# Kernel optimization log

Measured on AMD Instinct MI355X. Metric: run time of the kernel, lower is better.

## Reference

```python
import jax, jax.numpy as jnp
import numpy as np

B, P, PD = 32, 196, 768          # batch, n_subdivs, subdiv feature dim
D, H, L, NC = 768, 12, 8, 1000   # n_dims, n_heads, n_blocks, n_classes
HD = D // H                      # per-head dim (64)


def _pos_emb(n_pos, d):
    # faithful to _sinusoidal_positional_embeddings: row i (timestep) parity picks sin/cos
    i = jnp.arange(n_pos, dtype=jnp.float32)[:, None]
    j = jnp.arange(d, dtype=jnp.float32)[None, :]
    sin_v = jnp.sin(i / jnp.power(10000.0, j / d))
    cos_v = jnp.cos(i / jnp.power(10000.0, (j - 1.0) / d))
    return jnp.where((jnp.arange(n_pos)[:, None] % 2) == 0, sin_v, cos_v)  # (n_pos, d)


def _layernorm(x, g, b, eps=1e-5):
    m = jnp.mean(x, axis=-1, keepdims=True)
    v = jnp.var(x, axis=-1, keepdims=True)
    return (x - m) * jax.lax.rsqrt(v + eps) * g + b


def setup_inputs() -> dict:
    key = jax.random.key(0)
    ks = iter(jax.random.split(key, 16))
    nrm = lambda shape, s=0.02: jax.random.normal(next(ks), shape, jnp.float32) * s
    return {
        "x": jax.random.normal(next(ks), (B, P, PD), jnp.float32),
        "W_emb": nrm((PD, D)), "b_emb": jnp.zeros((D,), jnp.float32),
        "v_class": jax.random.uniform(next(ks), (1, D), jnp.float32),
        "ln1_g": jnp.ones((L, D), jnp.float32), "ln1_b": jnp.zeros((L, D), jnp.float32),
        "Wq": nrm((L, H, HD, HD)), "bq": jnp.zeros((L, H, HD), jnp.float32),
        "Wk": nrm((L, H, HD, HD)), "bk": jnp.zeros((L, H, HD), jnp.float32),
        "Wv": nrm((L, H, HD, HD)), "bv": jnp.zeros((L, H, HD), jnp.float32),
        "ln2_g": jnp.ones((L, D), jnp.float32), "ln2_b": jnp.zeros((L, D), jnp.float32),
        "W1": nrm((L, D, 4 * D)), "b1": jnp.zeros((L, 4 * D), jnp.float32),
        "W2": nrm((L, 4 * D, D)), "b2": jnp.zeros((L, D), jnp.float32),
        "W_cls": nrm((D, NC)), "b_cls": jnp.zeros((NC,), jnp.float32),
    }


def reference(x, W_emb, b_emb, v_class, ln1_g, ln1_b, Wq, bq, Wk, bk, Wv, bv,
              ln2_g, ln2_b, W1, b1, W2, b2, W_cls, b_cls):
    b = x.shape[0]
    pos = _pos_emb(P, D)                                  # (P, D), same for every sample
    h = x @ W_emb + b_emb + pos                           # (B, P, D)
    cls_tok = jnp.broadcast_to(v_class[None], (b, 1, D))
    h = jnp.concatenate([cls_tok, h], axis=1)             # (B, S, D), S = P + 1
    S = P + 1
    attns = []
    for l in range(L):
        # --- MHSA: each head reads only its own hd-slice of the input ---
        xn = _layernorm(h, ln1_g[l], ln1_b[l])
        xh = xn.reshape(b, S, H, HD)
        q = jnp.einsum('bshi,hij->bshj', xh, Wq[l]) + bq[l]
        k = jnp.einsum('bshi,hij->bshj', xh, Wk[l]) + bk[l]
        v = jnp.einsum('bshi,hij->bshj', xh, Wv[l]) + bv[l]
        scores = jnp.einsum('bqhj,bkhj->bhqk', q, k) / (HD ** 0.5)
        a = jax.nn.softmax(scores, axis=-1)               # (B, H, S, S)
        attns.append(jnp.mean(a, axis=1))                 # mean over heads, (B, S, S)
        o = jnp.einsum('bhqk,bkhj->bqhj', a, v).reshape(b, S, D)
        h = o + h                                         # residual 1
        # --- MLP ---
        xn2 = _layernorm(h, ln2_g[l], ln2_b[l])
        m = jax.nn.gelu(xn2 @ W1[l] + b1[l], approximate=False)
        h = m @ W2[l] + b2[l] + h                         # residual 2
    cls = h[:, 0]
    pred = jax.nn.softmax(cls @ W_cls + b_cls, axis=-1)   # (B, NC)
    return pred, jnp.stack(attns)                         # attns: (L, B, S, S)
```

## Files before the change

### kernel.cpp

```cpp
#include <hip/hip_runtime.h>
#include <cstdint>

typedef unsigned short u16;
typedef __attribute__((ext_vector_type(8))) short bf16x8;
typedef __attribute__((ext_vector_type(4))) float f32x4;

#define DEV static __device__ __forceinline__

#define BB 32
#define PP 196
#define DD 768
#define HH 12
#define HDD 64
#define SS 197
#define NTOK 6304
#define NTOKX 6272
#define NCLS 1000
#define DD4 3072
#define KPAD 224
#define NBH 384
#define NLAY 8

DEV u16 f2bf(float f){ unsigned u=__float_as_uint(f); u += 0x7FFFu + ((u>>16)&1u); return (u16)(u>>16); }
DEV float bf2f(u16 u){ return __uint_as_float(((unsigned)u)<<16); }

typedef __attribute__((address_space(1))) void gas1;
typedef __attribute__((address_space(3))) void las3;

DEV void gld16(const void* g, void* l){
  __builtin_amdgcn_global_load_lds((gas1*)(uintptr_t)g, (las3*)(unsigned)(uintptr_t)l, 16, 0, 0);
}

struct __align__(8) u16x4 { u16 x,y,z,w; };


__global__ void pos_kernel(float* __restrict__ pos){
  int idx = blockIdx.x*256 + threadIdx.x;
  if (idx >= PP*DD) return;
  int p = idx / DD, j = idx - p*DD;
  int odd = p & 1;
  float e = ((float)j - (float)odd) * (1.0f/(float)DD);
  float arg = (float)p / powf(10000.0f, e);
  pos[idx] = odd ? cosf(arg) : sinf(arg);
}

__global__ void f32_to_bf16_kernel(const float* __restrict__ in, u16* __restrict__ out, int n4){
  int i = blockIdx.x*256 + threadIdx.x;
  if (i >= n4) return;
  float4 v = reinterpret_cast<const float4*>(in)[i];
  u16x4 o = { f2bf(v.x), f2bf(v.y), f2bf(v.z), f2bf(v.w) };
  reinterpret_cast<u16x4*>(out)[i] = o;
}

__global__ void clstok_kernel(const float* __restrict__ vcls, float* __restrict__ h){
  int b = blockIdx.x;
  for (int i = threadIdx.x; i < DD; i += 256)
    h[(size_t)b*SS*DD + i] = vcls[i];
}

__global__ void transpose_kernel(const float* __restrict__ in, u16* __restrict__ out, int R, int C){
  __shared__ float tile[32][33];
  int bx = blockIdx.x*32, by = blockIdx.y*32;
  size_t zoff = (size_t)blockIdx.z * R * C;
  const float* src = in + zoff;
  u16* dst = out + zoff;
  int tx = threadIdx.x, ty = threadIdx.y;
  #pragma unroll
  for (int q=0;q<4;q++)
    tile[ty + q*8][tx] = src[(size_t)(by + ty + q*8)*C + bx + tx];
  __syncthreads();
  #pragma unroll
  for (int q=0;q<4;q++)
    dst[(size_t)(bx + ty + q*8)*R + by + tx] = f2bf(tile[tx][ty + q*8]);
}

__global__ void ln_kernel(const float* __restrict__ h, const float* __restrict__ g,
                          const float* __restrict__ b, u16* __restrict__ xn){
  int t = blockIdx.x*4 + (threadIdx.x>>6);
  int lane = threadIdx.x & 63;
  const float4* src = reinterpret_cast<const float4*>(h + (size_t)t*DD);
  float4 xv[3];
  float s = 0.f, s2 = 0.f;
  #pragma unroll
  for (int p=0;p<3;p++){
    xv[p] = src[p*64 + lane];
    s  += xv[p].x + xv[p].y + xv[p].z + xv[p].w;
    s2 += xv[p].x*xv[p].x + xv[p].y*xv[p].y + xv[p].z*xv[p].z + xv[p].w*xv[p].w;
  }
  #pragma unroll
  for (int o=32;o>0;o>>=1){ s += __shfl_xor(s,o); s2 += __shfl_xor(s2,o); }
  float mean = s * (1.f/(float)DD);
  float rstd = rsqrtf(s2*(1.f/(float)DD) - mean*mean + 1e-5f);
  #pragma unroll
  for (int p=0;p<3;p++){
    int base = p*256 + lane*4;
    u16x4 o4 = { f2bf((xv[p].x-mean)*rstd*g[base+0]+b[base+0]),
                 f2bf((xv[p].y-mean)*rstd*g[base+1]+b[base+1]),
                 f2bf((xv[p].z-mean)*rstd*g[base+2]+b[base+2]),
                 f2bf((xv[p].w-mean)*rstd*g[base+3]+b[base+3]) };
    *reinterpret_cast<u16x4*>(&xn[(size_t)t*DD + base]) = o4;
  }
}

template<int EPI>
__global__ __launch_bounds__(256) void gemm_bf16(
    const u16* __restrict__ A, const u16* __restrict__ BT, int M, int K,
    int nbm, int nbn,
    const float* __restrict__ bias, const float* __restrict__ pos,
    float* __restrict__ Hout, u16* __restrict__ Bout)
{
  __shared__ __align__(16) u16 As[3][128*32];
  __shared__ __align__(16) u16 Bs[3][128*32];
  const int tid = threadIdx.x;
  const int wave = tid>>6, lane = tid&63;

  const int nwg = nbm*nbn;
  const int wg = blockIdx.x;
  const int xcd = wg & 7, ii = wg >> 3;
  const int q8 = nwg >> 3, r8 = nwg & 7;
  const int lin = (xcd < r8 ? xcd*(q8+1) : r8*(q8+1) + (xcd-r8)*q8) + ii;
  const int bm = lin / nbn, bn = lin - bm*nbn;

  const int wr = wave>>1, wc = wave&1;

  f32x4 acc[4][4] = {};

  const int lr = lane>>2;
  const int lc = ((lane&3) ^ ((lane>>3)&3)) * 8;
  int ar0 = bm*128 + (wave*2+0)*16 + lr; if (ar0 > M-1) ar0 = M-1;
  int ar1 = bm*128 + (wave*2+1)*16 + lr; if (ar1 > M-1) ar1 = M-1;
  const u16* aS0 = A + (size_t)ar0*K + lc;
  const u16* aS1 = A + (size_t)ar1*K + lc;
  const u16* bS0 = BT + (size_t)(bn*128 + (wave*2+0)*16 + lr)*K + lc;
  const u16* bS1 = BT + (size_t)(bn*128 + (wave*2+1)*16 + lr)*K + lc;
  const int d0 = (wave*2+0)*512;
  const int d1 = (wave*2+1)*512;

  auto stage = [&](int buf, int kt){
    gld16(aS0 + kt, &As[buf][d0]);
    gld16(aS1 + kt, &As[buf][d1]);
    gld16(bS0 + kt, &Bs[buf][d0]);
    gld16(bS1 + kt, &Bs[buf][d1]);
  };
  const int rchunk = ((lane>>4) ^ (((lane&15)>>1)&3)) * 8;
  auto compute = [&](int buf){
    bf16x8 af[4], bfv[4];
    #pragma unroll
    for (int i=0;i<4;i++)
      af[i] = *reinterpret_cast<const bf16x8*>(&As[buf][(wr*64 + i*16 + (lane&15))*32 + rchunk]);
    #pragma unroll
    for (int j=0;j<4;j++)
      bfv[j] = *reinterpret_cast<const bf16x8*>(&Bs[buf][(wc*64 + j*16 + (lane&15))*32 + rchunk]);
    #pragma unroll
    for (int i=0;i<4;i++)
      #pragma unroll
      for (int j=0;j<4;j++)
        acc[i][j] = __builtin_amdgcn_mfma_f32_16x16x32_bf16(af[i], bfv[j], acc[i][j], 0, 0, 0);
  };

  const int NT = K >> 5;
  stage(0, 0);
  stage(1, 32);
  for (int t = 0; t < NT-2; ++t){
    asm volatile("s_waitcnt vmcnt(4)" ::: "memory");
    __builtin_amdgcn_s_barrier();
    __builtin_amdgcn_sched_barrier(0);
    stage((t+2)%3, (t+2)*32);
    compute(t%3);
  }
  asm volatile("s_waitcnt vmcnt(4)" ::: "memory");
  __builtin_amdgcn_s_barrier();
  __builtin_amdgcn_sched_barrier(0);
  compute((NT-2)%3);
  asm volatile("s_waitcnt vmcnt(0)" ::: "memory");
  __builtin_amdgcn_s_barrier();
  __builtin_amdgcn_sched_barrier(0);
  compute((NT-1)%3);

  const int rowb = bm*128 + wr*64 + (lane>>4)*4;
  const int colb = bn*128 + wc*64 + (lane&15);
  const int Nst = nbn * 128;
  #pragma unroll
  for (int i=0;i<4;i++){
    #pragma unroll
    for (int j=0;j<4;j++){
      int col = colb + j*16;
      #pragma unroll
      for (int r=0;r<4;r++){
        int row = rowb + i*16 + r;
        if (row >= M) continue;
        float v = acc[i][j][r];
        if (EPI == 0){
          int bb = row / PP, p = row - bb*PP;
          Hout[((size_t)(bb*SS + 1 + p))*DD + col] = v + bias[col] + pos[p*DD + col];
        } else if (EPI == 1){
          float xg = v + bias[col];
          Bout[(size_t)row*Nst + col] = f2bf(0.5f*xg*(1.f + erff(xg*0.7071067811865475f)));
        } else {
          Hout[(size_t)row*DD + col] += v + bias[col];
        }
      }
    }
  }
}

__global__ __launch_bounds__(256) void qkv_kernel(
    const u16* __restrict__ xn,
    const u16* __restrict__ WqT, const u16* __restrict__ WkT, const u16* __restrict__ WvT,
    const float* __restrict__ bq, const float* __restrict__ bk, const float* __restrict__ bv,
    u16* __restrict__ qb, u16* __restrict__ kb, u16* __restrict__ vb)
{
  const int LDA = 72;
  __shared__ __align__(16) u16 Asm[128*72];
  __shared__ __align__(16) u16 Wsm[3][64*72];
  const int tid = threadIdx.x, wave = tid>>6, lane = tid&63;
  const int bm = blockIdx.x, hd = blockIdx.y;

  #pragma unroll
  for (int ps=0; ps<4; ++ps){
    int e = (ps*256 + tid)*8;
    int row = e>>6, col = e&63;
    int gr = bm*128 + row; if (gr > NTOK-1) gr = NTOK-1;
    *reinterpret_cast<int4*>(&Asm[row*LDA + col]) =
        *reinterpret_cast<const int4*>(&xn[(size_t)gr*DD + hd*HDD + col]);
  }
  const u16* wsrc[3] = { WqT + hd*4096, WkT + hd*4096, WvT + hd*4096 };
  #pragma unroll
  for (int w=0; w<3; ++w)
    #pragma unroll
    for (int ps=0; ps<2; ++ps){
      int e = (ps*256 + tid)*8;
      int row = e>>6, col = e&63;
      *reinterpret_cast<int4*>(&Wsm[w][row*LDA + col]) =
          *reinterpret_cast<const int4*>(&wsrc[w][row*64 + col]);
    }
  __syncthreads();

  bf16x8 af[2][2];
  #pragma unroll
  for (int i=0;i<2;i++)
    #pragma unroll
    for (int kk=0;kk<2;kk++)
      af[i][kk] = *reinterpret_cast<const bf16x8*>(&Asm[(wave*32 + i*16 + (lane&15))*LDA + kk*32 + (lane>>4)*8]);

  f32x4 acc[3][2][4] = {};
  #pragma unroll
  for (int w=0;w<3;w++)
    #pragma unroll
    for (int kk=0;kk<2;kk++)
      #pragma unroll
      for (int j=0;j<4;j++){
        bf16x8 bfv = *reinterpret_cast<const bf16x8*>(&Wsm[w][(j*16 + (lane&15))*LDA + kk*32 + (lane>>4)*8]);
        #pragma unroll
        for (int i=0;i<2;i++)
          acc[w][i][j] = __builtin_amdgcn_mfma_f32_16x16x32_bf16(af[i][kk], bfv, acc[w][i][j], 0,0,0);
      }

  const float* bqh = bq + hd*HDD;
  const float* bkh = bk + hd*HDD;
  const float* bvh = bv + hd*HDD;
  #pragma unroll
  for (int i=0;i<2;i++)
    #pragma unroll
    for (int j=0;j<4;j++){
      int d = j*16 + (lane&15);
      #pragma unroll
      for (int r=0;r<4;r++){
        int t = bm*128 + wave*32 + i*16 + (lane>>4)*4 + r;
        if (t >= NTOK) continue;
        int b = t / SS, sx = t - b*SS;
        size_t bh = (size_t)b*HH + hd;
        qb[(bh*SS + sx)*HDD + d] = f2bf(acc[0][i][j][r] + bqh[d]);
        kb[(bh*SS + sx)*HDD + d] = f2bf(acc[1][i][j][r] + bkh[d]);
        vb[(bh*KPAD + sx)*HDD + d] = f2bf(acc[2][i][j][r] + bvh[d]);
      }
    }
}

__global__ __launch_bounds__(256) void scores_kernel(
    const u16* __restrict__ qb, const u16* __restrict__ kb, u16* __restrict__ sc)
{
  const int LDA = 72;
  __shared__ __align__(16) u16 Qs[128*72];
  __shared__ __align__(16) u16 Ks[128*72];
  const int tid = threadIdx.x, wave = tid>>6, lane = tid&63;
  const int bm = blockIdx.x, bn = blockIdx.y, bh = blockIdx.z;
  #pragma unroll
  for (int ps=0; ps<4; ++ps){
    int e = (ps*256 + tid)*8;
    int row = e>>6, col = e&63;
    int qr = bm*128 + row; if (qr > SS-1) qr = SS-1;
    int kr = bn*128 + row; if (kr > SS-1) kr = SS-1;
    *reinterpret_cast<int4*>(&Qs[row*LDA + col]) = *reinterpret_cast<const int4*>(&qb[((size_t)bh*SS + qr)*HDD + col]);
    *reinterpret_cast<int4*>(&Ks[row*LDA + col]) = *reinterpret_cast<const int4*>(&kb[((size_t)bh*SS + kr)*HDD + col]);
  }
  __syncthreads();
  const int wr = wave>>1, wc = wave&1;
  f32x4 acc[4][4] = {};
  #pragma unroll
  for (int kk=0;kk<2;kk++){
    bf16x8 af[4], bfv[4];
    #pragma unroll
    for (int i=0;i<4;i++) af[i] = *reinterpret_cast<const bf16x8*>(&Qs[(wr*64+i*16+(lane&15))*LDA + kk*32 + (lane>>4)*8]);
    #pragma unroll
    for (int j=0;j<4;j++) bfv[j] = *reinterpret_cast<const bf16x8*>(&Ks[(wc*64+j*16+(lane&15))*LDA + kk*32 + (lane>>4)*8]);
    #pragma unroll
    for (int i=0;i<4;i++)
      #pragma unroll
      for (int j=0;j<4;j++)
        acc[i][j] = __builtin_amdgcn_mfma_f32_16x16x32_bf16(af[i], bfv[j], acc[i][j], 0,0,0);
  }
  #pragma unroll
  for (int i=0;i<4;i++)
    #pragma unroll
    for (int j=0;j<4;j++){
      int kg = bn*128 + wc*64 + j*16 + (lane&15);
      #pragma unroll
      for (int r=0;r<4;r++){
        int qg = bm*128 + wr*64 + i*16 + (lane>>4)*4 + r;
        if (qg < SS && kg < SS)
          sc[((size_t)bh*SS + qg)*KPAD + kg] = f2bf(acc[i][j][r] * 0.125f);
      }
    }
}

__global__ void softmax_kernel(u16* __restrict__ sc){
  int row = blockIdx.x*4 + (threadIdx.x>>6);
  int lane = threadIdx.x & 63;
  u16* src = sc + (size_t)row*KPAD;
  float v[4]; float mx = -1e30f;
  #pragma unroll
  for (int p=0;p<4;p++){
    int c = lane + p*64;
    v[p] = (c < SS) ? bf2f(src[c]) : -1e30f;
    mx = fmaxf(mx, v[p]);
  }
  #pragma unroll
  for (int o=32;o>0;o>>=1) mx = fmaxf(mx, __shfl_xor(mx,o));
  float s = 0.f;
  #pragma unroll
  for (int p=0;p<4;p++){
    int c = lane + p*64;
    v[p] = (c < SS) ? expf(v[p]-mx) : 0.f;
    s += v[p];
  }
  #pragma unroll
  for (int o=32;o>0;o>>=1) s += __shfl_xor(s,o);
  float inv = 1.f / s;
  #pragma unroll
  for (int p=0;p<4;p++){
    int c = lane + p*64;
    if (c < KPAD) src[c] = f2bf((c < SS) ? v[p]*inv : 0.f);
  }
}

__global__ void attnmean_kernel(const u16* __restrict__ attn, float* __restrict__ outp){
  int qi = blockIdx.x, b = blockIdx.y, kk = threadIdx.x;
  if (kk >= SS) return;
  float s = 0.f;
  #pragma unroll
  for (int h=0; h<HH; ++h)
    s += bf2f(attn[(((size_t)b*HH + h)*SS + qi)*KPAD + kk]);
  outp[((size_t)b*SS + qi)*SS + kk] = s * (1.f/12.f);
}

__global__ __launch_bounds__(256) void av_kernel(
    const u16* __restrict__ attn, const u16* __restrict__ vb, float* __restrict__ h)
{
  const int LDA = 40;
  const int LDB = 40;
  __shared__ __align__(16) u16 Asm[128*40];
  __shared__ __align__(16) u16 Bsm[64*40];
  const int tid = threadIdx.x, wave = tid>>6, lane = tid&63;
  const int bm = blockIdx.x, bh = blockIdx.y;
  const int b = bh / HH, hd = bh - b*HH;
  f32x4 acc[2][4] = {};
  for (int k0 = 0; k0 < KPAD; k0 += 32){
    if (k0) __syncthreads();
    #pragma unroll
    for (int ps=0; ps<2; ++ps){
      int e = (ps*256 + tid)*8;
      int row = e>>5, col = e&31;
      int ar = bm*128 + row; if (ar > SS-1) ar = SS-1;
      *reinterpret_cast<int4*>(&Asm[row*LDA + col]) =
          *reinterpret_cast<const int4*>(&attn[((size_t)bh*SS + ar)*KPAD + k0 + col]);
    }
    {
      int kk = tid>>3;
      int d0 = (tid&7)*8;
      bf16x8 vv = *reinterpret_cast<const bf16x8*>(&vb[((size_t)bh*KPAD + k0 + kk)*HDD + d0]);
      #pragma unroll
      for (int q=0;q<8;q++) Bsm[(d0+q)*LDB + kk] = (u16)vv[q];
    }
    __syncthreads();
    bf16x8 af[2], bfv[4];
    #pragma unroll
    for (int i=0;i<2;i++) af[i] = *reinterpret_cast<const bf16x8*>(&Asm[(wave*32 + i*16 + (lane&15))*LDA + (lane>>4)*8]);
    #pragma unroll
    for (int j=0;j<4;j++) bfv[j] = *reinterpret_cast<const bf16x8*>(&Bsm[(j*16 + (lane&15))*LDB + (lane>>4)*8]);
    #pragma unroll
    for (int i=0;i<2;i++)
      #pragma unroll
      for (int j=0;j<4;j++)
        acc[i][j] = __builtin_amdgcn_mfma_f32_16x16x32_bf16(af[i], bfv[j], acc[i][j], 0,0,0);
  }
  #pragma unroll
  for (int i=0;i<2;i++)
    #pragma unroll
    for (int j=0;j<4;j++){
      int d = j*16 + (lane&15);
      #pragma unroll
      for (int r=0;r<4;r++){
        int sx = bm*128 + wave*32 + i*16 + (lane>>4)*4 + r;
        if (sx < SS)
          h[((size_t)b*SS + sx)*DD + hd*HDD + d] += acc[i][j][r];
      }
    }
}

__global__ __launch_bounds__(256) void logits_kernel(
    const float* __restrict__ h, const float* __restrict__ Wc,
    const float* __restrict__ bc, float* __restrict__ logits)
{
  __shared__ float xs[DD];
  const int b = blockIdx.x, tid = threadIdx.x;
  for (int i = tid; i < DD; i += 256) xs[i] = h[(size_t)b*SS*DD + i];
  __syncthreads();
  const int c = blockIdx.y*250 + tid;
  if (tid >= 250 || c >= NCLS) return;
  float acc = bc[c];
  const float* wcol = Wc + c;
  #pragma unroll 16
  for (int k = 0; k < DD; ++k)
    acc += xs[k] * wcol[(size_t)k*NCLS];
  logits[(size_t)b*NCLS + c] = acc;
}

__global__ __launch_bounds__(256) void pred_softmax_kernel(
    const float* __restrict__ logits, float* __restrict__ outp)
{
  __shared__ float red[256];
  const int b = blockIdx.x, tid = threadIdx.x;
  float acc[4], mx = -1e30f;
  #pragma unroll
  for (int m=0;m<4;m++){
    int c = tid + m*256;
    acc[m] = (c < NCLS) ? logits[(size_t)b*NCLS + c] : -1e30f;
    mx = fmaxf(mx, acc[m]);
  }
  red[tid] = mx; __syncthreads();
  for (int o=128;o>0;o>>=1){ if (tid<o) red[tid] = fmaxf(red[tid], red[tid+o]); __syncthreads(); }
  mx = red[0]; __syncthreads();
  float ex[4]; float s = 0.f;
  #pragma unroll
  for (int m=0;m<4;m++){
    int c = tid + m*256;
    ex[m] = (c < NCLS) ? expf(acc[m]-mx) : 0.f;
    s += ex[m];
  }
  red[tid] = s; __syncthreads();
  for (int o=128;o>0;o>>=1){ if (tid<o) red[tid] += red[tid+o]; __syncthreads(); }
  float inv = 1.f / red[0];
  #pragma unroll
  for (int m=0;m<4;m++){
    int c = tid + m*256;
    if (c < NCLS) outp[(size_t)b*NCLS + c] = ex[m]*inv;
  }
}

extern "C" void kernel_launch(void* const* d_in, const int* in_sizes, int n_in,
                              void* d_out, int out_size, void* d_ws, size_t ws_size,
                              hipStream_t stream)
{
  const float* x      = (const float*)d_in[0];
  const float* W_emb  = (const float*)d_in[1];
  const float* b_emb  = (const float*)d_in[2];
  const float* v_class= (const float*)d_in[3];
  const float* ln1_g  = (const float*)d_in[4];
  const float* ln1_b  = (const float*)d_in[5];
  const float* Wq     = (const float*)d_in[6];
  const float* bq     = (const float*)d_in[7];
  const float* Wk     = (const float*)d_in[8];
  const float* bk     = (const float*)d_in[9];
  const float* Wv     = (const float*)d_in[10];
  const float* bv     = (const float*)d_in[11];
  const float* ln2_g  = (const float*)d_in[12];
  const float* ln2_b  = (const float*)d_in[13];
  const float* W1     = (const float*)d_in[14];
  const float* b1     = (const float*)d_in[15];
  const float* W2     = (const float*)d_in[16];
  const float* b2     = (const float*)d_in[17];
  const float* W_cls  = (const float*)d_in[18];
  const float* b_cls  = (const float*)d_in[19];
  (void)in_sizes; (void)n_in; (void)out_size;
  float* outp = (float*)d_out;

  char* ws = (char*)d_ws;
  size_t off = 0;
  auto alloc = [&](size_t bytes)->char*{
    char* p = ws + off;
    off = (off + bytes + 255) & ~((size_t)255);
    return p;
  };
  float* pos    = (float*)alloc((size_t)PP*DD*4);
  float* hbuf   = (float*)alloc((size_t)NTOK*DD*4);
  u16*   xnb    = (u16*)  alloc((size_t)NTOK*DD*2);
  u16*   WembT  = (u16*)  alloc((size_t)DD*DD*2);
  u16*   W1Tall = (u16*)  alloc((size_t)NLAY*DD*DD4*2);
  u16*   W2Tall = (u16*)  alloc((size_t)NLAY*DD*DD4*2);
  u16*   WqT    = (u16*)  alloc((size_t)NLAY*HH*HDD*HDD*2);
  u16*   WkT    = (u16*)  alloc((size_t)NLAY*HH*HDD*HDD*2);
  u16*   WvT    = (u16*)  alloc((size_t)NLAY*HH*HDD*HDD*2);
  char*  blob   = alloc((size_t)NTOK*DD4*2);
  float* logitsb= (float*)alloc((size_t)BB*NCLS*4);
  u16* qbuf = (u16*)blob;
  u16* kbuf = qbuf + (size_t)NBH*SS*HDD;
  u16* vbuf = kbuf + (size_t)NBH*SS*HDD;
  u16* scb  = vbuf + (size_t)NBH*KPAD*HDD;
  u16* mbuf = (u16*)blob;
  u16* xbf  = scb;
  if (ws_size < off) return;

  hipMemsetAsync(vbuf, 0, (size_t)NBH*KPAD*HDD*2, stream);
  pos_kernel<<<(PP*DD+255)/256, 256, 0, stream>>>(pos);
  f32_to_bf16_kernel<<<(NTOKX*DD/4+255)/256, 256, 0, stream>>>(x, xbf, NTOKX*DD/4);
  dim3 tb(32,8);
  transpose_kernel<<<dim3(DD/32, DD/32, 1), tb, 0, stream>>>(W_emb, WembT, DD, DD);
  transpose_kernel<<<dim3(2,2,NLAY*HH), tb, 0, stream>>>(Wq, WqT, HDD, HDD);
  transpose_kernel<<<dim3(2,2,NLAY*HH), tb, 0, stream>>>(Wk, WkT, HDD, HDD);
  transpose_kernel<<<dim3(2,2,NLAY*HH), tb, 0, stream>>>(Wv, WvT, HDD, HDD);
  transpose_kernel<<<dim3(DD4/32, DD/32, NLAY), tb, 0, stream>>>(W1, W1Tall, DD, DD4);
  transpose_kernel<<<dim3(DD/32, DD4/32, NLAY), tb, 0, stream>>>(W2, W2Tall, DD4, DD);

  gemm_bf16<0><<<49*6, 256, 0, stream>>>(xbf, WembT, NTOKX, DD, 49, 6, b_emb, pos, hbuf, nullptr);
  clstok_kernel<<<BB, 256, 0, stream>>>(v_class, hbuf);

  for (int l=0; l<NLAY; ++l){
    ln_kernel<<<NTOK/4, 256, 0, stream>>>(hbuf, ln1_g + l*DD, ln1_b + l*DD, xnb);
    qkv_kernel<<<dim3(50, HH), 256, 0, stream>>>(xnb,
        WqT + (size_t)l*HH*4096, WkT + (size_t)l*HH*4096, WvT + (size_t)l*HH*4096,
        bq + l*HH*HDD, bk + l*HH*HDD, bv + l*HH*HDD, qbuf, kbuf, vbuf);
    scores_kernel<<<dim3(2,2,NBH), 256, 0, stream>>>(qbuf, kbuf, scb);
    softmax_kernel<<<NBH*SS/4, 256, 0, stream>>>(scb);
    attnmean_kernel<<<dim3(SS, BB), 256, 0, stream>>>(scb, outp + 32000 + (size_t)l*BB*SS*SS);
    av_kernel<<<dim3(2, NBH), 256, 0, stream>>>(scb, vbuf, hbuf);
    ln_kernel<<<NTOK/4, 256, 0, stream>>>(hbuf, ln2_g + l*DD, ln2_b + l*DD, xnb);
    gemm_bf16<1><<<50*24, 256, 0, stream>>>(xnb, W1Tall + (size_t)l*DD*DD4, NTOK, DD, 50, 24,
                                            b1 + l*DD4, nullptr, nullptr, mbuf);
    gemm_bf16<2><<<50*6, 256, 0, stream>>>(mbuf, W2Tall + (size_t)l*DD*DD4, NTOK, DD4, 50, 6,
                                           b2 + l*DD, nullptr, hbuf, nullptr);
  }
  logits_kernel<<<dim3(BB, 4), 256, 0, stream>>>(hbuf, W_cls, b_cls, logitsb);
  pred_softmax_kernel<<<BB, 256, 0, stream>>>(logitsb, outp);
}
```

Measured before the change: 1.957 ms.

## Fuse attention scores with softmax and switch GEMM to double-buffered LDS

The separate scores and softmax kernels are merged into one kernel. Each workgroup loads all 197 keys, computes a full row band of QK^T in registers, and applies softmax with intra-quad shuffles before writing bf16 probabilities once. This removes a bf16 round trip of the score matrix and a launch per layer. Separately, the generic GEMM goes from a 3-stage LDS pipeline to 2-stage double buffering with an extra barrier per K step. That lowers LDS use and may raise occupancy, but it risks less latency hiding.

```diff
diff --git a/kernel.cpp b/kernel.cpp
--- a/kernel.cpp
+++ b/kernel.cpp
@@ -109,8 +109,8 @@
     const float* __restrict__ bias, const float* __restrict__ pos,
     float* __restrict__ Hout, u16* __restrict__ Bout)
 {
-  __shared__ __align__(16) u16 As[3][128*32];
-  __shared__ __align__(16) u16 Bs[3][128*32];
+  __shared__ __align__(16) u16 As[2][128*32];
+  __shared__ __align__(16) u16 Bs[2][128*32];
   const int tid = threadIdx.x;
   const int wave = tid>>6, lane = tid&63;
 
@@ -160,22 +160,20 @@
 
   const int NT = K >> 5;
   stage(0, 0);
-  stage(1, 32);
-  for (int t = 0; t < NT-2; ++t){
-    asm volatile("s_waitcnt vmcnt(4)" ::: "memory");
+  int cur = 0;
+  for (int t = 0; t < NT; ++t){
+    if (t+1 < NT){
+      stage(cur^1, (t+1)*32);
+      asm volatile("s_waitcnt vmcnt(4)" ::: "memory");
+    } else {
+      asm volatile("s_waitcnt vmcnt(0)" ::: "memory");
+    }
     __builtin_amdgcn_s_barrier();
     __builtin_amdgcn_sched_barrier(0);
-    stage((t+2)%3, (t+2)*32);
-    compute(t%3);
-  }
-  asm volatile("s_waitcnt vmcnt(4)" ::: "memory");
-  __builtin_amdgcn_s_barrier();
-  __builtin_amdgcn_sched_barrier(0);
-  compute((NT-2)%3);
-  asm volatile("s_waitcnt vmcnt(0)" ::: "memory");
-  __builtin_amdgcn_s_barrier();
-  __builtin_amdgcn_sched_barrier(0);
-  compute((NT-1)%3);
+    compute(cur);
+    __builtin_amdgcn_s_barrier();
+    cur ^= 1;
+  }
 
   const int rowb = bm*128 + wr*64 + (lane>>4)*4;
   const int colb = bn*128 + wc*64 + (lane&15);
@@ -277,80 +275,91 @@
     }
 }
 
-__global__ __launch_bounds__(256) void scores_kernel(
-    const u16* __restrict__ qb, const u16* __restrict__ kb, u16* __restrict__ sc)
+__global__ __launch_bounds__(256) void attn_scores_softmax_kernel(
+    const u16* __restrict__ qb, const u16* __restrict__ kb, u16* __restrict__ attn)
 {
   const int LDA = 72;
   __shared__ __align__(16) u16 Qs[128*72];
-  __shared__ __align__(16) u16 Ks[128*72];
+  __shared__ __align__(16) u16 Ks[KPAD*72];
   const int tid = threadIdx.x, wave = tid>>6, lane = tid&63;
-  const int bm = blockIdx.x, bn = blockIdx.y, bh = blockIdx.z;
+  const int bm = blockIdx.x, bh = blockIdx.y;
+
   #pragma unroll
   for (int ps=0; ps<4; ++ps){
     int e = (ps*256 + tid)*8;
     int row = e>>6, col = e&63;
     int qr = bm*128 + row; if (qr > SS-1) qr = SS-1;
-    int kr = bn*128 + row; if (kr > SS-1) kr = SS-1;
-    *reinterpret_cast<int4*>(&Qs[row*LDA + col]) = *reinterpret_cast<const int4*>(&qb[((size_t)bh*SS + qr)*HDD + col]);
-    *reinterpret_cast<int4*>(&Ks[row*LDA + col]) = *reinterpret_cast<const int4*>(&kb[((size_t)bh*SS + kr)*HDD + col]);
+    *reinterpret_cast<int4*>(&Qs[row*LDA + col]) =
+        *reinterpret_cast<const int4*>(&qb[((size_t)bh*SS + qr)*HDD + col]);
+  }
+  #pragma unroll
+  for (int ps=0; ps<7; ++ps){
+    int e = (ps*256 + tid)*8;
+    int row = e>>6, col = e&63;
+    int kr = row; if (kr > SS-1) kr = SS-1;
+    *reinterpret_cast<int4*>(&Ks[row*LDA + col]) =
+        *reinterpret_cast<const int4*>(&kb[((size_t)bh*SS + kr)*HDD + col]);
   }
   __syncthreads();
-  const int wr = wave>>1, wc = wave&1;
-  f32x4 acc[4][4] = {};
-  #pragma unroll
-  for (int kk=0;kk<2;kk++){
-    bf16x8 af[4], bfv[4];
-    #pragma unroll
-    for (int i=0;i<4;i++) af[i] = *reinterpret_cast<const bf16x8*>(&Qs[(wr*64+i*16+(lane&15))*LDA + kk*32 + (lane>>4)*8]);
-    #pragma unroll
-    for (int j=0;j<4;j++) bfv[j] = *reinterpret_cast<const bf16x8*>(&Ks[(wc*64+j*16+(lane&15))*LDA + kk*32 + (lane>>4)*8]);
-    #pragma unroll
-    for (int i=0;i<4;i++)
-      #pragma unroll
-      for (int j=0;j<4;j++)
-        acc[i][j] = __builtin_amdgcn_mfma_f32_16x16x32_bf16(af[i], bfv[j], acc[i][j], 0,0,0);
-  }
-  #pragma unroll
-  for (int i=0;i<4;i++)
-    #pragma unroll
-    for (int j=0;j<4;j++){
-      int kg = bn*128 + wc*64 + j*16 + (lane&15);
-      #pragma unroll
-      for (int r=0;r<4;r++){
-        int qg = bm*128 + wr*64 + i*16 + (lane>>4)*4 + r;
-        if (qg < SS && kg < SS)
-          sc[((size_t)bh*SS + qg)*KPAD + kg] = f2bf(acc[i][j][r] * 0.125f);
-      }
-    }
-}
-
-__global__ void softmax_kernel(u16* __restrict__ sc){
-  int row = blockIdx.x*4 + (threadIdx.x>>6);
-  int lane = threadIdx.x & 63;
-  u16* src = sc + (size_t)row*KPAD;
-  float v[4]; float mx = -1e30f;
-  #pragma unroll
-  for (int p=0;p<4;p++){
-    int c = lane + p*64;
-    v[p] = (c < SS) ? bf2f(src[c]) : -1e30f;
-    mx = fmaxf(mx, v[p]);
-  }
-  #pragma unroll
-  for (int o=32;o>0;o>>=1) mx = fmaxf(mx, __shfl_xor(mx,o));
-  float s = 0.f;
-  #pragma unroll
-  for (int p=0;p<4;p++){
-    int c = lane + p*64;
-    v[p] = (c < SS) ? expf(v[p]-mx) : 0.f;
-    s += v[p];
-  }
-  #pragma unroll
-  for (int o=32;o>0;o>>=1) s += __shfl_xor(s,o);
-  float inv = 1.f / s;
-  #pragma unroll
-  for (int p=0;p<4;p++){
-    int c = lane + p*64;
-    if (c < KPAD) src[c] = f2bf((c < SS) ? v[p]*inv : 0.f);
+
+  bf16x8 af[2][2];
+  #pragma unroll
+  for (int i=0;i<2;i++)
+    #pragma unroll
+    for (int kk=0;kk<2;kk++)
+      af[i][kk] = *reinterpret_cast<const bf16x8*>(&Qs[(wave*32 + i*16 + (lane&15))*LDA + kk*32 + (lane>>4)*8]);
+
+  f32x4 acc[2][14];
+  #pragma unroll
+  for (int i=0;i<2;i++)
+    #pragma unroll
+    for (int j=0;j<14;j++)
+      acc[i][j] = f32x4{0.f,0.f,0.f,0.f};
+
+  #pragma unroll
+  for (int kk=0;kk<2;kk++)
+    #pragma unroll
+    for (int j=0;j<14;j++){
+      bf16x8 bfv = *reinterpret_cast<const bf16x8*>(&Ks[(j*16 + (lane&15))*LDA + kk*32 + (lane>>4)*8]);
+      #pragma unroll
+      for (int i=0;i<2;i++)
+        acc[i][j] = __builtin_amdgcn_mfma_f32_16x16x32_bf16(af[i][kk], bfv, acc[i][j], 0,0,0);
+    }
+
+  const int kcol = lane & 15;
+  #pragma unroll
+  for (int i=0;i<2;i++){
+    #pragma unroll
+    for (int r=0;r<4;r++){
+      int qg = bm*128 + wave*32 + i*16 + (lane>>4)*4 + r;
+      float vals[14];
+      float mx = -1e30f;
+      #pragma unroll
+      for (int j=0;j<14;j++){
+        int kg = j*16 + kcol;
+        float v = (kg < SS) ? acc[i][j][r]*0.125f : -1e30f;
+        vals[j] = v;
+        mx = fmaxf(mx, v);
+      }
+      mx = fmaxf(mx, __shfl_xor(mx,1)); mx = fmaxf(mx, __shfl_xor(mx,2));
+      mx = fmaxf(mx, __shfl_xor(mx,4)); mx = fmaxf(mx, __shfl_xor(mx,8));
+      float s = 0.f;
+      #pragma unroll
+      for (int j=0;j<14;j++){
+        int kg = j*16 + kcol;
+        float e = (kg < SS) ? expf(vals[j]-mx) : 0.f;
+        vals[j] = e; s += e;
+      }
+      s += __shfl_xor(s,1); s += __shfl_xor(s,2);
+      s += __shfl_xor(s,4); s += __shfl_xor(s,8);
+      float inv = 1.f / s;
+      if (qg < SS){
+        u16* dst = attn + ((size_t)bh*SS + qg)*KPAD;
+        #pragma unroll
+        for (int j=0;j<14;j++)
+          dst[j*16 + kcol] = f2bf(vals[j]*inv);
+      }
+    }
   }
 }
 
@@ -540,8 +549,7 @@
     qkv_kernel<<<dim3(50, HH), 256, 0, stream>>>(xnb,
         WqT + (size_t)l*HH*4096, WkT + (size_t)l*HH*4096, WvT + (size_t)l*HH*4096,
         bq + l*HH*HDD, bk + l*HH*HDD, bv + l*HH*HDD, qbuf, kbuf, vbuf);
-    scores_kernel<<<dim3(2,2,NBH), 256, 0, stream>>>(qbuf, kbuf, scb);
-    softmax_kernel<<<NBH*SS/4, 256, 0, stream>>>(scb);
+    attn_scores_softmax_kernel<<<dim3(2, NBH), 256, 0, stream>>>(qbuf, kbuf, scb);
     attnmean_kernel<<<dim3(SS, BB), 256, 0, stream>>>(scb, outp + 32000 + (size_t)l*BB*SS*SS);
     av_kernel<<<dim3(2, NBH), 256, 0, stream>>>(scb, vbuf, hbuf);
     ln_kernel<<<NTOK/4, 256, 0, stream>>>(hbuf, ln2_g + l*DD, ln2_b + l*DD, xnb);
```

After: 1.855 ms. -5.2%, faster.
